# Optimization experiments

Measured on AMD Instinct MI355X. Metric: run time of the kernel, lower is better.

The kernel has to match this reference:

```python
import jax, jax.numpy as jnp
import numpy as np

RESOLUTIONS = [16, 18, 20, 22, 24, 27, 30, 34, 38, 42, 47, 52, 58, 64, 72, 80]
NUM_LEVELS = 16
C_IN = 16
C_OUT = 16
K = 3


def setup_inputs() -> dict:
    key = jax.random.key(0)
    k_in, k_w, k_b = jax.random.split(key, 3)
    res = np.asarray(RESOLUTIONS, dtype=np.int32)
    offsets = np.concatenate([[0], np.cumsum(res.astype(np.int64) ** 3)]).astype(np.int32)
    N = int(offsets[-1])  # 1,844,282 total embeddings across all levels
    B = 2
    return {
        "input": jax.random.normal(k_in, (B, N, C_IN), dtype=jnp.float32),
        "weight": 0.01 * jax.random.normal(k_w, (NUM_LEVELS, K, K, K, C_IN, C_OUT), dtype=jnp.float32),
        "bias": 0.01 * jax.random.normal(k_b, (NUM_LEVELS, C_OUT), dtype=jnp.float32),
        "offsets": jnp.asarray(offsets),
        "resolutions": jnp.asarray(res),
    }


def _conv_levels(input, weight, bias, off, res):
    # input: (B, N, C_in). Each level l occupies input[:, off[l]:off[l+1]] and is a
    # dense R_l^3 grid (row-major x,y,z) since R^3 <= hashmap_size for all levels.
    # Per-level 3D conv (zero padding outside the grid) with per-level weight+bias.
    B, _, Cin = input.shape
    outs = []
    for l in range(len(res)):
        R = int(res[l])
        x = input[:, int(off[l]):int(off[l + 1])].reshape(B, R, R, R, Cin)
        y = jax.lax.conv_general_dilated(
            x, weight[l], window_strides=(1, 1, 1), padding="SAME",
            dimension_numbers=("NDHWC", "DHWIO", "NDHWC"))
        y = y + bias[l]  # (B, R, R, R, C_out)
        outs.append(y.reshape(B, R * R * R, -1))
    return jnp.concatenate(outs, axis=1)  # (B, N, C_out)


def reference(input, weight, bias, offsets, resolutions):
    off = np.asarray(offsets)
    res = np.asarray(resolutions)
    return _conv_levels(input, weight, bias, off, res)
```

## Files before the change

kernel.cpp:

```cpp
#include <hip/hip_runtime.h>


#define NLEV 16
#define NTOT 1844282

typedef short  short8 __attribute__((ext_vector_type(8)));
typedef float  f32x4  __attribute__((ext_vector_type(4)));

__constant__ int c_res[NLEV]  = {16,18,20,22,24,27,30,34,38,42,47,52,58,64,72,80};
__constant__ int c_voff[NLEV] = {0,4096,9928,17928,28576,42400,62083,89083,
                                 128387,183259,257347,361170,501778,696890,
                                 959034,1332282};
__constant__ int c_tblk[NLEV+1] = {0,16,66,116,188,260,358,486,729,1029,1392,
                                   1824,2500,3400,4424,6044,8044};
__constant__ int c_ntz[NLEV] = {1,2,2,2,2,2,2,3,3,3,3,4,4,4,5,5};
__constant__ int c_nty[NLEV] = {4,5,5,6,6,7,8,9,10,11,12,13,15,16,18,20};

__device__ __forceinline__ unsigned short f2bf(float f) {
    union { float f; unsigned int u; } v; v.f = f;
    unsigned int u = v.u;
    return (unsigned short)((u + 0x7FFFu + ((u >> 16) & 1u)) >> 16);
}

__device__ __forceinline__ short8 lds_load8(const short* p) {
    return *reinterpret_cast<const short8*>(__builtin_assume_aligned(p, 16));
}
__device__ __forceinline__ void lds_store8(short* p, short8 v) {
    *reinterpret_cast<short8*>(__builtin_assume_aligned(p, 16)) = v;
}

__global__ __launch_bounds__(256, 3)
void conv3d_mfma_kernel(const float* __restrict__ in,
                        const float* __restrict__ w,
                        const float* __restrict__ bias,
                        float* __restrict__ out) {
    __shared__ __align__(16) short s_in[648 * 24];

    const int bid = blockIdx.x;
    const int b   = blockIdx.y;

    int l = 0;
#pragma unroll
    for (int i = 1; i < NLEV; ++i) l += (bid >= c_tblk[i]);

    const int R    = c_res[l];
    const int voff = c_voff[l];
    const int ntz  = c_ntz[l];
    const int nty  = c_nty[l];

    const int local = bid - c_tblk[l];
    const int tz = local % ntz;
    const int t2 = local / ntz;
    const int ty = t2 % nty;
    const int tx = t2 / nty;

    const float* inb  = in  + ((long long)b * NTOT + voff) * 16;
    float*       outb = out + ((long long)b * NTOT + voff) * 16;

    for (int h = threadIdx.x; h < 648; h += 256) {
        const int hz = h % 18;
        const int t  = h / 18;
        const int hy = t % 6;
        const int hx = t / 6;
        const int gx = tx * 4 - 1 + hx;
        const int gy = ty * 4 - 1 + hy;
        const int gz = tz * 16 - 1 + hz;
        const bool ok = ((unsigned)gx < (unsigned)R) &
                        ((unsigned)gy < (unsigned)R) &
                        ((unsigned)gz < (unsigned)R);
        short v[16];
        if (ok) {
            const float4* ip = reinterpret_cast<const float4*>(
                inb + (long long)((gx * R + gy) * R + gz) * 16);
#pragma unroll
            for (int g = 0; g < 4; ++g) {
                float4 q = ip[g];
                v[g * 4 + 0] = (short)f2bf(q.x);
                v[g * 4 + 1] = (short)f2bf(q.y);
                v[g * 4 + 2] = (short)f2bf(q.z);
                v[g * 4 + 3] = (short)f2bf(q.w);
            }
        } else {
#pragma unroll
            for (int g = 0; g < 16; ++g) v[g] = 0;
        }
        short8 lo, hi;
#pragma unroll
        for (int g = 0; g < 8; ++g) { lo[g] = v[g]; hi[g] = v[8 + g]; }
        lds_store8(&s_in[h * 24], lo);
        lds_store8(&s_in[h * 24 + 8], hi);
    }

    const int lane = threadIdx.x & 63;
    const int wv   = threadIdx.x >> 6;
    const int quad = lane >> 4;
    const int m    = lane & 15;
    const int co   = m;
    const int h8   = (quad & 1) * 8;
    const int qh   = quad >> 1;

    const float* wlev = w + l * 6912;
    const float  bv   = bias[l * 16 + co];

    int    ofs[14];
    short8 wf[14];
#pragma unroll
    for (int i = 0; i < 14; ++i) {
        const int t  = 2 * i + qh;
        const int ta = t > 26 ? 26 : t;
        const int kd = ta / 9;
        const int rr = ta - kd * 9;
        const int kh = rr / 3;
        const int kw = rr - kh * 3;
        ofs[i] = ((kd * 6 + kh) * 18 + kw + m) * 24 + h8;
        short8 wv8;
        if (t < 27) {
            const float* wp = wlev + t * 256 + h8 * 16 + co;
#pragma unroll
            for (int j = 0; j < 8; ++j) wv8[j] = (short)f2bf(wp[j * 16]);
        } else {
#pragma unroll
            for (int j = 0; j < 8; ++j) wv8[j] = 0;
        }
        wf[i] = wv8;
    }

    __syncthreads();

    const int gx = tx * 4 + wv;
    if (gx < R) {
        const int pb0 = wv * 2592;
#pragma unroll
        for (int j = 0; j < 4; ++j) {
            const int gy = ty * 4 + j;
            if (gy < R) {
                f32x4 acc = {bv, bv, bv, bv};
                const int pb = pb0 + j * 432;
#pragma unroll
                for (int i = 0; i < 14; ++i) {
                    short8 a = lds_load8(&s_in[pb + ofs[i]]);
                    acc = __builtin_amdgcn_mfma_f32_16x16x32_bf16(a, wf[i], acc, 0, 0, 0);
                }
                float* ob = outb + (long long)(gx * R + gy) * R * 16 + co;
                const int gz0 = tz * 16 + quad * 4;
#pragma unroll
                for (int r = 0; r < 4; ++r) {
                    const int gz = gz0 + r;
                    if (gz < R) ob[(long long)gz * 16] = acc[r];
                }
            }
        }
    }
}

extern "C" void kernel_launch(void* const* d_in, const int* in_sizes, int n_in,
                              void* d_out, int out_size, void* d_ws, size_t ws_size,
                              hipStream_t stream) {
    const float* in   = (const float*)d_in[0];
    const float* w    = (const float*)d_in[1];
    const float* bias = (const float*)d_in[2];
    float* out = (float*)d_out;

    dim3 grid(8044, 2);
    conv3d_mfma_kernel<<<grid, 256, 0, stream>>>(in, w, bias, out);
}
```

Before: 486.5 us.

## Prepack bf16 weight fragments in a pre-kernel and use hardware packed bf16 convert

Adds a small pre-pass kernel that converts the per-level weights to bf16 and lays them out in MFMA fragment order in workspace, so each block loads its 14 weight fragments with vector loads instead of 112 strided scalar loads plus conversions. The input halo conversion switches to the packed v_cvt_pk_bf16_f32 instruction, and tap offsets become compile-time constants selected by qh. Occupancy hint is raised from 3 to 4 blocks per CU. This adds an extra kernel launch per call, and the hardware convert's rounding may differ slightly from the software round-to-nearest-even.

```diff
diff --git a/kernel.cpp b/kernel.cpp
--- a/kernel.cpp
+++ b/kernel.cpp
@@ -6,6 +6,7 @@
 
 typedef short  short8 __attribute__((ext_vector_type(8)));
 typedef float  f32x4  __attribute__((ext_vector_type(4)));
+typedef unsigned int u32x4 __attribute__((ext_vector_type(4)));
 
 __constant__ int c_res[NLEV]  = {16,18,20,22,24,27,30,34,38,42,47,52,58,64,72,80};
 __constant__ int c_voff[NLEV] = {0,4096,9928,17928,28576,42400,62083,89083,
@@ -22,16 +23,50 @@
     return (unsigned short)((u + 0x7FFFu + ((u >> 16) & 1u)) >> 16);
 }
 
+__device__ __forceinline__ unsigned int cvt_pk_bf16(float lo, float hi) {
+    unsigned int r;
+    asm("v_cvt_pk_bf16_f32 %0, %1, %2" : "=v"(r) : "v"(lo), "v"(hi));
+    return r;
+}
+
+constexpr int geo24(int t) {
+    int ta = t > 26 ? 26 : t;
+    int kd = ta / 9, rr = ta - kd * 9, kh = rr / 3, kw = rr - kh * 3;
+    return ((kd * 6 + kh) * 18 + kw) * 24;
+}
+
 __device__ __forceinline__ short8 lds_load8(const short* p) {
     return *reinterpret_cast<const short8*>(__builtin_assume_aligned(p, 16));
 }
-__device__ __forceinline__ void lds_store8(short* p, short8 v) {
-    *reinterpret_cast<short8*>(__builtin_assume_aligned(p, 16)) = v;
+
+__global__ void pack_weights(const float* __restrict__ w,
+                             unsigned short* __restrict__ wbuf) {
+    const int l = blockIdx.x;
+    const float* wlev = w + l * 6912;
+    for (int task = threadIdx.x; task < 14 * 64; task += blockDim.x) {
+        const int i    = task >> 6;
+        const int lane = task & 63;
+        const int quad = lane >> 4;
+        const int m    = lane & 15;
+        const int h8   = (quad & 1) * 8;
+        const int qh   = quad >> 1;
+        const int t    = 2 * i + qh;
+        short8 v;
+        if (t < 27) {
+            const float* wp = wlev + t * 256 + h8 * 16 + m;
+#pragma unroll
+            for (int j = 0; j < 8; ++j) v[j] = (short)f2bf(wp[j * 16]);
+        } else {
+#pragma unroll
+            for (int j = 0; j < 8; ++j) v[j] = 0;
+        }
+        *reinterpret_cast<short8*>(wbuf + l * 7168 + task * 8) = v;
+    }
 }
 
-__global__ __launch_bounds__(256, 3)
+__global__ __launch_bounds__(256, 4)
 void conv3d_mfma_kernel(const float* __restrict__ in,
-                        const float* __restrict__ w,
+                        const unsigned short* __restrict__ wbuf,
                         const float* __restrict__ bias,
                         float* __restrict__ out) {
     __shared__ __align__(16) short s_in[648 * 24];
@@ -68,27 +103,22 @@
         const bool ok = ((unsigned)gx < (unsigned)R) &
                         ((unsigned)gy < (unsigned)R) &
                         ((unsigned)gz < (unsigned)R);
-        short v[16];
+        u32x4 lo = {0u, 0u, 0u, 0u}, hi = {0u, 0u, 0u, 0u};
         if (ok) {
-            const float4* ip = reinterpret_cast<const float4*>(
-                inb + (long long)((gx * R + gy) * R + gz) * 16);
-#pragma unroll
-            for (int g = 0; g < 4; ++g) {
-                float4 q = ip[g];
-                v[g * 4 + 0] = (short)f2bf(q.x);
-                v[g * 4 + 1] = (short)f2bf(q.y);
-                v[g * 4 + 2] = (short)f2bf(q.z);
-                v[g * 4 + 3] = (short)f2bf(q.w);
-            }
-        } else {
-#pragma unroll
-            for (int g = 0; g < 16; ++g) v[g] = 0;
+            const f32x4* ip = reinterpret_cast<const f32x4*>(
+                inb + (long long)(((gx * R + gy) * R + gz) * 16));
+            f32x4 q0 = ip[0], q1 = ip[1], q2 = ip[2], q3 = ip[3];
+            lo[0] = cvt_pk_bf16(q0[0], q0[1]);
+            lo[1] = cvt_pk_bf16(q0[2], q0[3]);
+            lo[2] = cvt_pk_bf16(q1[0], q1[1]);
+            lo[3] = cvt_pk_bf16(q1[2], q1[3]);
+            hi[0] = cvt_pk_bf16(q2[0], q2[1]);
+            hi[1] = cvt_pk_bf16(q2[2], q2[3]);
+            hi[2] = cvt_pk_bf16(q3[0], q3[1]);
+            hi[3] = cvt_pk_bf16(q3[2], q3[3]);
         }
-        short8 lo, hi;
-#pragma unroll
-        for (int g = 0; g < 8; ++g) { lo[g] = v[g]; hi[g] = v[8 + g]; }
-        lds_store8(&s_in[h * 24], lo);
-        lds_store8(&s_in[h * 24 + 8], hi);
+        *reinterpret_cast<u32x4*>(&s_in[h * 24])     = lo;
+        *reinterpret_cast<u32x4*>(&s_in[h * 24 + 8]) = hi;
     }
 
     const int lane = threadIdx.x & 63;
@@ -99,31 +129,18 @@
     const int h8   = (quad & 1) * 8;
     const int qh   = quad >> 1;
 
-    const float* wlev = w + l * 6912;
-    const float  bv   = bias[l * 16 + co];
+    const float bv = bias[l * 16 + co];
 
-    int    ofs[14];
     short8 wf[14];
+    const short8* wp8 = reinterpret_cast<const short8*>(wbuf) + l * 896 + lane;
 #pragma unroll
-    for (int i = 0; i < 14; ++i) {
-        const int t  = 2 * i + qh;
-        const int ta = t > 26 ? 26 : t;
-        const int kd = ta / 9;
-        const int rr = ta - kd * 9;
-        const int kh = rr / 3;
-        const int kw = rr - kh * 3;
-        ofs[i] = ((kd * 6 + kh) * 18 + kw + m) * 24 + h8;
-        short8 wv8;
-        if (t < 27) {
-            const float* wp = wlev + t * 256 + h8 * 16 + co;
+    for (int i = 0; i < 14; ++i) wf[i] = wp8[i * 64];
+
+    const int mbase = m * 24 + h8;
+    int ofs[14];
 #pragma unroll
-            for (int j = 0; j < 8; ++j) wv8[j] = (short)f2bf(wp[j * 16]);
-        } else {
-#pragma unroll
-            for (int j = 0; j < 8; ++j) wv8[j] = 0;
-        }
-        wf[i] = wv8;
-    }
+    for (int i = 0; i < 14; ++i)
+        ofs[i] = (qh ? geo24(2 * i + 1) : geo24(2 * i)) + mbase;
 
     __syncthreads();
 
@@ -160,7 +177,9 @@
     const float* w    = (const float*)d_in[1];
     const float* bias = (const float*)d_in[2];
     float* out = (float*)d_out;
+    unsigned short* wbuf = (unsigned short*)d_ws;
 
+    pack_weights<<<dim3(NLEV), 256, 0, stream>>>(w, wbuf);
     dim3 grid(8044, 2);
-    conv3d_mfma_kernel<<<grid, 256, 0, stream>>>(in, w, bias, out);
+    conv3d_mfma_kernel<<<grid, 256, 0, stream>>>(in, wbuf, bias, out);
 }
```

New measurement: 436.1 us. -10.4%, faster.
